# Optimization experiments

Hardware: AMD Instinct MI355X
Metric: run time of the kernel (lower is better)

The kernel has to match this reference:

```python
import jax, jax.numpy as jnp
import numpy as np

THETA = 10000.0
R_TOK = 4  # region_token_num


def _local_positions(regions, max_n):
    # 0-based position of each token within its region (count of prior tokens
    # with the same region id) -- order-based, works for any region layout.
    onehot = jax.nn.one_hot(regions, max_n + 1, dtype=jnp.int32)  # [B,T,N+1]
    counts = jnp.cumsum(onehot, axis=1)                            # inclusive
    return jnp.take_along_axis(counts, regions[..., None], axis=-1)[..., 0] - 1


def _rope(q, k, pos, theta):
    # full-head-dim rotary embedding, split-half convention
    D = q.shape[-1]
    inv_freq = 1.0 / (theta ** (jnp.arange(0, D, 2, dtype=jnp.float32) / D))  # [D/2]
    ang = pos[..., None].astype(jnp.float32) * inv_freq                        # [B,S,D/2]
    cos = jnp.tile(jnp.cos(ang), (1, 1, 2))[:, None]                           # [B,1,S,D]
    sin = jnp.tile(jnp.sin(ang), (1, 1, 2))[:, None]

    def rot(x):
        h = x.shape[-1] // 2
        return jnp.concatenate([-x[..., h:], x[..., :h]], axis=-1)

    return q * cos + rot(q) * sin, k * cos + rot(k) * sin


def setup_inputs() -> dict:
    B, H, D = 2, 16, 64
    T, MAX_N = 2048, 64
    P = MAX_N * R_TOK
    key = jax.random.key(0)
    ks = jax.random.split(key, 7)
    f = lambda k, s: jax.random.normal(k, s, dtype=jnp.float32)
    regions = jnp.sort(jax.random.randint(ks[6], (B, T), 1, MAX_N + 1, dtype=jnp.int32), axis=-1)
    return {
        'pool_q': f(ks[0], (B, H, P, D)),
        'pool_k': f(ks[1], (B, H, P, D)),
        'pool_v': f(ks[2], (B, H, P, D)),
        'x_q': f(ks[3], (B, H, T, D)),
        'x_k': f(ks[4], (B, H, T, D)),
        'x_v': f(ks[5], (B, H, T, D)),
        'regions': regions,
        't_mask': jnp.ones((B, T), dtype=bool),
        'n_mask': jnp.ones((B, MAX_N), dtype=bool),
        'max_n': MAX_N,
    }


def reference(pool_q, pool_k, pool_v, x_q, x_k, x_v, regions, t_mask, n_mask, max_n):
    B, H, P, D = pool_q.shape
    R = R_TOK
    # sequence = [pool, x]
    q = jnp.concatenate([pool_q, x_q], axis=2)
    k = jnp.concatenate([pool_k, x_k], axis=2)
    v = jnp.concatenate([pool_v, x_v], axis=2)

    # local-mode positions (use_pool_offset=False -> pool tokens at pos 0)
    pool_pos = jnp.zeros((B, P), dtype=jnp.int32)
    x_pos = (_local_positions(regions, max_n) + R) * (regions > 0).astype(jnp.int32)
    pos = jnp.concatenate([pool_pos, x_pos], axis=-1)  # [B,S]
    q, k = _rope(q, k, pos, THETA)

    # block-local (same-region) mask: [B,1,S,S], True = allowed
    pool_region = jnp.broadcast_to(jnp.repeat(jnp.arange(1, max_n + 1, dtype=jnp.int32), R)[None], (B, P))
    pool_valid = jnp.repeat(n_mask, R, axis=1)                      # [B,P]
    full_region = jnp.concatenate([pool_region, regions], axis=-1)  # [B,S]
    full_valid = jnp.concatenate([pool_valid, t_mask], axis=-1)     # [B,S]
    same = full_region[:, :, None] == full_region[:, None, :]
    valid = full_valid[:, :, None] & full_valid[:, None, :]
    nonpad = (full_region != 0)[:, :, None] & (full_region != 0)[:, None, :]
    mask = (same & valid & nonpad)[:, None]                          # [B,1,S,S]

    scores = jnp.einsum('bhqd,bhkd->bhqk', q, k) / jnp.sqrt(jnp.float32(D))
    scores = jnp.where(mask, scores, jnp.float32(-1e9))
    attn = jax.nn.softmax(scores, axis=-1)
    out = jnp.einsum('bhqk,bhkd->bhqd', attn, v)
    return out[:, :, :P, :]
```

## Files before the change

### kernel.cpp

```cpp
#include <hip/hip_runtime.h>

#define BB   2
#define HH   16
#define DD   64
#define TT   2048
#define MAXN 64
#define RTOK 4
#define PP   (MAXN * RTOK)
#define STR  72

typedef unsigned short u16x8 __attribute__((ext_vector_type(8)));
typedef unsigned short u16x4 __attribute__((ext_vector_type(4)));

__device__ __forceinline__ unsigned short f2bf(float f) {
    unsigned u = __float_as_uint(f);
    u += 0x7FFFu + ((u >> 16) & 1u);
    return (unsigned short)(u >> 16);
}
__device__ __forceinline__ float bf2f(unsigned short u) {
    return __uint_as_float(((unsigned int)u) << 16);
}

__global__ __launch_bounds__(256)
void build_ranges(const int* __restrict__ regions, int* __restrict__ tab) {
    const int b   = blockIdx.x;
    const int tid = threadIdx.x;
    const int* reg = regions + b * TT;
    int* t = tab + b * 66;
    const int i0 = tid * 8;
    int v[9];
    const int4 a0 = *(const int4*)(reg + i0);
    const int4 a1 = *(const int4*)(reg + i0 + 4);
    v[0] = a0.x; v[1] = a0.y; v[2] = a0.z; v[3] = a0.w;
    v[4] = a1.x; v[5] = a1.y; v[6] = a1.z; v[7] = a1.w;
    v[8] = (tid == 255) ? (MAXN + 1) : reg[i0 + 8];
    if (tid == 0)
        for (int rr = 1; rr <= v[0]; ++rr) t[rr] = 0;
    #pragma unroll
    for (int j = 0; j < 8; ++j)
        for (int rr = v[j] + 1; rr <= v[j + 1]; ++rr) t[rr] = i0 + j + 1;
}

__global__ __launch_bounds__(64, 2)
void lapd_attn(const float* __restrict__ pool_q,
               const float* __restrict__ pool_k,
               const float* __restrict__ pool_v,
               const float* __restrict__ x_k,
               const float* __restrict__ x_v,
               const int* __restrict__ tab,
               float* __restrict__ out) {
    const int blk   = blockIdx.x;
    const int r_idx = blk & (MAXN - 1);
    const int bh    = blk >> 6;
    const int b     = bh / HH;
    const int lane  = threadIdx.x;

    __shared__ __align__(16) unsigned short k_s16[64][STR];
    __shared__ __align__(16) unsigned short v_t16[64][STR];
    __shared__ __align__(16) unsigned short p_s16[4][STR];
    __shared__ float q_s[4][DD];

    const int* tb    = tab + b * 66;
    const int start  = tb[r_idx + 1];
    const int cnt    = tb[r_idx + 2] - start;
    const int sstart = (cnt > 0) ? start : 0;

    const size_t poolbase = ((size_t)bh * PP + r_idx * RTOK) * DD;
    const float* pk = pool_k + poolbase;
    const float* pv = pool_v + poolbase;
    const float* xk = x_k + (size_t)bh * TT * DD;
    const float* xv = x_v + (size_t)bh * TT * DD;

    const int qr = lane >> 4;
    const int qc = (lane & 15) * 4;
    {
        const float4 q4 = *(const float4*)(pool_q + poolbase + (size_t)(qr * DD) + qc);
        *(float4*)&q_s[qr][qc] =
            make_float4(q4.x * 0.125f, q4.y * 0.125f, q4.z * 0.125f, q4.w * 0.125f);
    }

    const int g = lane >> 3;
    const int d = (lane & 7) * 4;
    float invf[4];
    #pragma unroll
    for (int c = 0; c < 4; ++c)
        invf[c] = __expf((float)(d + c) * (-9.210340371976184f / 32.0f));

    float a0 = 0, a1 = 0, a2 = 0, a3 = 0, l = 0;
    int xbase = 0;
    bool first = true;

    for (;;) {
        const int koff = first ? RTOK : 0;
        int nx = cnt - xbase;
        if (nx > 64 - koff) nx = 64 - koff;
        if (nx < 0) nx = 0;
        const int tn = koff + nx;

        __syncthreads();

        #pragma unroll
        for (int ph = 0; ph < 4; ++ph) {
            const int keyA = ph * 16 + 2 * g;
            const int keyB = keyA + 1;
            int xiA = keyA - koff; if (xiA > nx - 1) xiA = nx - 1; if (xiA < 0) xiA = 0;
            int xiB = keyB - koff; if (xiB > nx - 1) xiB = nx - 1; if (xiB < 0) xiB = 0;
            const bool pA = first && (keyA < RTOK);
            const bool pB = first && (keyB < RTOK);
            const float* kbA = pA ? (pk + keyA * DD) : (xk + (size_t)(sstart + xbase + xiA) * DD);
            const float* vbA = pA ? (pv + keyA * DD) : (xv + (size_t)(sstart + xbase + xiA) * DD);
            const float* kbB = pB ? (pk + keyB * DD) : (xk + (size_t)(sstart + xbase + xiB) * DD);
            const float* vbB = pB ? (pv + keyB * DD) : (xv + (size_t)(sstart + xbase + xiB) * DD);
            const float4 kA0 = *(const float4*)(kbA + d);
            const float4 kA1 = *(const float4*)(kbA + d + 32);
            const float4 vA0 = *(const float4*)(vbA + d);
            const float4 vA1 = *(const float4*)(vbA + d + 32);
            const float4 kB0 = *(const float4*)(kbB + d);
            const float4 kB1 = *(const float4*)(kbB + d + 32);
            const float4 vB0 = *(const float4*)(vbB + d);
            const float4 vB1 = *(const float4*)(vbB + d + 32);

            {
                float lo0 = kA0.x, lo1 = kA0.y, lo2 = kA0.z, lo3 = kA0.w;
                float hi0 = kA1.x, hi1 = kA1.y, hi2 = kA1.z, hi3 = kA1.w;
                if (!pA) {
                    const float pos = (float)(xbase + xiA + RTOK);
                    float sv, cv;
                    __sincosf(pos * invf[0], &sv, &cv);
                    { const float L = lo0, H = hi0; lo0 = L*cv - H*sv; hi0 = H*cv + L*sv; }
                    __sincosf(pos * invf[1], &sv, &cv);
                    { const float L = lo1, H = hi1; lo1 = L*cv - H*sv; hi1 = H*cv + L*sv; }
                    __sincosf(pos * invf[2], &sv, &cv);
                    { const float L = lo2, H = hi2; lo2 = L*cv - H*sv; hi2 = H*cv + L*sv; }
                    __sincosf(pos * invf[3], &sv, &cv);
                    { const float L = lo3, H = hi3; lo3 = L*cv - H*sv; hi3 = H*cv + L*sv; }
                }
                u16x4 wlo = {f2bf(lo0), f2bf(lo1), f2bf(lo2), f2bf(lo3)};
                u16x4 whi = {f2bf(hi0), f2bf(hi1), f2bf(hi2), f2bf(hi3)};
                *(u16x4*)&k_s16[keyA][d]      = wlo;
                *(u16x4*)&k_s16[keyA][d + 32] = whi;
            }
            {
                float lo0 = kB0.x, lo1 = kB0.y, lo2 = kB0.z, lo3 = kB0.w;
                float hi0 = kB1.x, hi1 = kB1.y, hi2 = kB1.z, hi3 = kB1.w;
                if (!pB) {
                    const float pos = (float)(xbase + xiB + RTOK);
                    float sv, cv;
                    __sincosf(pos * invf[0], &sv, &cv);
                    { const float L = lo0, H = hi0; lo0 = L*cv - H*sv; hi0 = H*cv + L*sv; }
                    __sincosf(pos * invf[1], &sv, &cv);
                    { const float L = lo1, H = hi1; lo1 = L*cv - H*sv; hi1 = H*cv + L*sv; }
                    __sincosf(pos * invf[2], &sv, &cv);
                    { const float L = lo2, H = hi2; lo2 = L*cv - H*sv; hi2 = H*cv + L*sv; }
                    __sincosf(pos * invf[3], &sv, &cv);
                    { const float L = lo3, H = hi3; lo3 = L*cv - H*sv; hi3 = H*cv + L*sv; }
                }
                u16x4 wlo = {f2bf(lo0), f2bf(lo1), f2bf(lo2), f2bf(lo3)};
                u16x4 whi = {f2bf(hi0), f2bf(hi1), f2bf(hi2), f2bf(hi3)};
                *(u16x4*)&k_s16[keyB][d]      = wlo;
                *(u16x4*)&k_s16[keyB][d + 32] = whi;
            }
            {
                const unsigned w0 = (unsigned)f2bf(vA0.x) | ((unsigned)f2bf(vB0.x) << 16);
                const unsigned w1 = (unsigned)f2bf(vA0.y) | ((unsigned)f2bf(vB0.y) << 16);
                const unsigned w2 = (unsigned)f2bf(vA0.z) | ((unsigned)f2bf(vB0.z) << 16);
                const unsigned w3 = (unsigned)f2bf(vA0.w) | ((unsigned)f2bf(vB0.w) << 16);
                const unsigned h0 = (unsigned)f2bf(vA1.x) | ((unsigned)f2bf(vB1.x) << 16);
                const unsigned h1 = (unsigned)f2bf(vA1.y) | ((unsigned)f2bf(vB1.y) << 16);
                const unsigned h2 = (unsigned)f2bf(vA1.z) | ((unsigned)f2bf(vB1.z) << 16);
                const unsigned h3 = (unsigned)f2bf(vA1.w) | ((unsigned)f2bf(vB1.w) << 16);
                *(unsigned*)&v_t16[d + 0][keyA]      = w0;
                *(unsigned*)&v_t16[d + 1][keyA]      = w1;
                *(unsigned*)&v_t16[d + 2][keyA]      = w2;
                *(unsigned*)&v_t16[d + 3][keyA]      = w3;
                *(unsigned*)&v_t16[d + 32][keyA]     = h0;
                *(unsigned*)&v_t16[d + 33][keyA]     = h1;
                *(unsigned*)&v_t16[d + 34][keyA]     = h2;
                *(unsigned*)&v_t16[d + 35][keyA]     = h3;
            }
        }
        __syncthreads();

        float s0 = 0, s1 = 0, s2 = 0, s3 = 0;
        #pragma unroll
        for (int dd2 = 0; dd2 < DD; dd2 += 8) {
            const u16x8 kk = *(const u16x8*)&k_s16[lane][dd2];
            const float k0 = bf2f(kk[0]), k1 = bf2f(kk[1]), k2 = bf2f(kk[2]), k3 = bf2f(kk[3]);
            const float k4 = bf2f(kk[4]), k5 = bf2f(kk[5]), k6 = bf2f(kk[6]), k7 = bf2f(kk[7]);
            const float4 qa0 = *(const float4*)&q_s[0][dd2];
            const float4 qb0 = *(const float4*)&q_s[0][dd2 + 4];
            const float4 qa1 = *(const float4*)&q_s[1][dd2];
            const float4 qb1 = *(const float4*)&q_s[1][dd2 + 4];
            const float4 qa2 = *(const float4*)&q_s[2][dd2];
            const float4 qb2 = *(const float4*)&q_s[2][dd2 + 4];
            const float4 qa3 = *(const float4*)&q_s[3][dd2];
            const float4 qb3 = *(const float4*)&q_s[3][dd2 + 4];
            s0 += qa0.x*k0 + qa0.y*k1 + qa0.z*k2 + qa0.w*k3 + qb0.x*k4 + qb0.y*k5 + qb0.z*k6 + qb0.w*k7;
            s1 += qa1.x*k0 + qa1.y*k1 + qa1.z*k2 + qa1.w*k3 + qb1.x*k4 + qb1.y*k5 + qb1.z*k6 + qb1.w*k7;
            s2 += qa2.x*k0 + qa2.y*k1 + qa2.z*k2 + qa2.w*k3 + qb2.x*k4 + qb2.y*k5 + qb2.z*k6 + qb2.w*k7;
            s3 += qa3.x*k0 + qa3.y*k1 + qa3.z*k2 + qa3.w*k3 + qb3.x*k4 + qb3.y*k5 + qb3.z*k6 + qb3.w*k7;
        }
        const bool ok = (lane < tn);
        p_s16[0][lane] = f2bf(ok ? __expf(s0) : 0.0f);
        p_s16[1][lane] = f2bf(ok ? __expf(s1) : 0.0f);
        p_s16[2][lane] = f2bf(ok ? __expf(s2) : 0.0f);
        p_s16[3][lane] = f2bf(ok ? __expf(s3) : 0.0f);
        __syncthreads();

        #pragma unroll
        for (int k = 0; k < 64; k += 8) {
            const u16x8 pp = *(const u16x8*)&p_s16[qr][k];
            const float p0 = bf2f(pp[0]), p1 = bf2f(pp[1]), p2 = bf2f(pp[2]), p3 = bf2f(pp[3]);
            const float p4 = bf2f(pp[4]), p5 = bf2f(pp[5]), p6 = bf2f(pp[6]), p7 = bf2f(pp[7]);
            const u16x8 w0 = *(const u16x8*)&v_t16[qc + 0][k];
            const u16x8 w1 = *(const u16x8*)&v_t16[qc + 1][k];
            const u16x8 w2 = *(const u16x8*)&v_t16[qc + 2][k];
            const u16x8 w3 = *(const u16x8*)&v_t16[qc + 3][k];
            a0 += p0*bf2f(w0[0]) + p1*bf2f(w0[1]) + p2*bf2f(w0[2]) + p3*bf2f(w0[3])
                + p4*bf2f(w0[4]) + p5*bf2f(w0[5]) + p6*bf2f(w0[6]) + p7*bf2f(w0[7]);
            a1 += p0*bf2f(w1[0]) + p1*bf2f(w1[1]) + p2*bf2f(w1[2]) + p3*bf2f(w1[3])
                + p4*bf2f(w1[4]) + p5*bf2f(w1[5]) + p6*bf2f(w1[6]) + p7*bf2f(w1[7]);
            a2 += p0*bf2f(w2[0]) + p1*bf2f(w2[1]) + p2*bf2f(w2[2]) + p3*bf2f(w2[3])
                + p4*bf2f(w2[4]) + p5*bf2f(w2[5]) + p6*bf2f(w2[6]) + p7*bf2f(w2[7]);
            a3 += p0*bf2f(w3[0]) + p1*bf2f(w3[1]) + p2*bf2f(w3[2]) + p3*bf2f(w3[3])
                + p4*bf2f(w3[4]) + p5*bf2f(w3[5]) + p6*bf2f(w3[6]) + p7*bf2f(w3[7]);
            l  += ((p0 + p1) + (p2 + p3)) + ((p4 + p5) + (p6 + p7));
        }

        xbase += nx;
        first = false;
        if (xbase >= cnt) break;
    }

    const float rl = 1.0f / l;
    *(float4*)(out + poolbase + (size_t)(qr * DD) + qc) =
        make_float4(a0 * rl, a1 * rl, a2 * rl, a3 * rl);
}

extern "C" void kernel_launch(void* const* d_in, const int* in_sizes, int n_in,
                              void* d_out, int out_size, void* d_ws, size_t ws_size,
                              hipStream_t stream) {
    const float* pool_q  = (const float*)d_in[0];
    const float* pool_k  = (const float*)d_in[1];
    const float* pool_v  = (const float*)d_in[2];
    const float* x_k     = (const float*)d_in[4];
    const float* x_v     = (const float*)d_in[5];
    const int*   regions = (const int*)d_in[6];
    float*       out     = (float*)d_out;
    int*         tab     = (int*)d_ws;

    build_ranges<<<dim3(BB), dim3(256), 0, stream>>>(regions, tab);
    lapd_attn<<<dim3(BB * HH * MAXN), dim3(64), 0, stream>>>(
        pool_q, pool_k, pool_v, x_k, x_v, tab, out);
}
```

Before: 110.8 us.

## Split region attention across two waves and skip empty key chunks

Each block now runs two waves of 64 lanes instead of one. Key and value loading is split so each wave handles half of the 64-key chunk. The QK dot product is split across half-lanes over the head dimension and combined with a shuffle. The PV loop runs only up to the rounded-up valid key count, and each thread produces two output columns instead of four. This aims to cut per-thread serial work and skip padding keys, since regions average about 32 tokens. The cost is an extra shuffle and a larger block.

Result: faster. 107.8 us (-2.8%).

```diff
diff --git a/kernel.cpp b/kernel.cpp
--- a/kernel.cpp
+++ b/kernel.cpp
@@ -41,7 +41,7 @@
         for (int rr = v[j] + 1; rr <= v[j + 1]; ++rr) t[rr] = i0 + j + 1;
 }
 
-__global__ __launch_bounds__(64, 2)
+__global__ __launch_bounds__(128, 4)
 void lapd_attn(const float* __restrict__ pool_q,
                const float* __restrict__ pool_k,
                const float* __restrict__ pool_v,
@@ -53,7 +53,9 @@
     const int r_idx = blk & (MAXN - 1);
     const int bh    = blk >> 6;
     const int b     = bh / HH;
-    const int lane  = threadIdx.x;
+    const int tid   = threadIdx.x;
+    const int wave  = tid >> 6;
+    const int lane  = tid & 63;
 
     __shared__ __align__(16) unsigned short k_s16[64][STR];
     __shared__ __align__(16) unsigned short v_t16[64][STR];
@@ -71,11 +73,10 @@
     const float* xk = x_k + (size_t)bh * TT * DD;
     const float* xv = x_v + (size_t)bh * TT * DD;
 
-    const int qr = lane >> 4;
-    const int qc = (lane & 15) * 4;
     {
-        const float4 q4 = *(const float4*)(pool_q + poolbase + (size_t)(qr * DD) + qc);
-        *(float4*)&q_s[qr][qc] =
+        const int r = lane >> 4, c = (lane & 15) * 4;
+        const float4 q4 = *(const float4*)(pool_q + poolbase + (size_t)(r * DD) + c);
+        *(float4*)&q_s[r][c] =
             make_float4(q4.x * 0.125f, q4.y * 0.125f, q4.z * 0.125f, q4.w * 0.125f);
     }
 
@@ -86,7 +87,12 @@
     for (int c = 0; c < 4; ++c)
         invf[c] = __expf((float)(d + c) * (-9.210340371976184f / 32.0f));
 
-    float a0 = 0, a1 = 0, a2 = 0, a3 = 0, l = 0;
+    const int sk = lane & 31;
+    const int h  = lane >> 5;
+    const int row = 2 * wave + (lane >> 5);
+    const int dp  = (lane & 31) * 2;
+
+    float accA = 0.0f, accB = 0.0f, l = 0.0f;
     int xbase = 0;
     bool first = true;
 
@@ -95,136 +101,142 @@
         int nx = cnt - xbase;
         if (nx > 64 - koff) nx = 64 - koff;
         if (nx < 0) nx = 0;
-        const int tn = koff + nx;
+        const int tn   = koff + nx;
+        const int kmax = (tn + 7) & ~7;
 
         __syncthreads();
 
         #pragma unroll
-        for (int ph = 0; ph < 4; ++ph) {
-            const int keyA = ph * 16 + 2 * g;
-            const int keyB = keyA + 1;
-            int xiA = keyA - koff; if (xiA > nx - 1) xiA = nx - 1; if (xiA < 0) xiA = 0;
-            int xiB = keyB - koff; if (xiB > nx - 1) xiB = nx - 1; if (xiB < 0) xiB = 0;
-            const bool pA = first && (keyA < RTOK);
-            const bool pB = first && (keyB < RTOK);
-            const float* kbA = pA ? (pk + keyA * DD) : (xk + (size_t)(sstart + xbase + xiA) * DD);
-            const float* vbA = pA ? (pv + keyA * DD) : (xv + (size_t)(sstart + xbase + xiA) * DD);
-            const float* kbB = pB ? (pk + keyB * DD) : (xk + (size_t)(sstart + xbase + xiB) * DD);
-            const float* vbB = pB ? (pv + keyB * DD) : (xv + (size_t)(sstart + xbase + xiB) * DD);
-            const float4 kA0 = *(const float4*)(kbA + d);
-            const float4 kA1 = *(const float4*)(kbA + d + 32);
-            const float4 vA0 = *(const float4*)(vbA + d);
-            const float4 vA1 = *(const float4*)(vbA + d + 32);
-            const float4 kB0 = *(const float4*)(kbB + d);
-            const float4 kB1 = *(const float4*)(kbB + d + 32);
-            const float4 vB0 = *(const float4*)(vbB + d);
-            const float4 vB1 = *(const float4*)(vbB + d + 32);
-
-            {
-                float lo0 = kA0.x, lo1 = kA0.y, lo2 = kA0.z, lo3 = kA0.w;
-                float hi0 = kA1.x, hi1 = kA1.y, hi2 = kA1.z, hi3 = kA1.w;
-                if (!pA) {
-                    const float pos = (float)(xbase + xiA + RTOK);
-                    float sv, cv;
-                    __sincosf(pos * invf[0], &sv, &cv);
-                    { const float L = lo0, H = hi0; lo0 = L*cv - H*sv; hi0 = H*cv + L*sv; }
-                    __sincosf(pos * invf[1], &sv, &cv);
-                    { const float L = lo1, H = hi1; lo1 = L*cv - H*sv; hi1 = H*cv + L*sv; }
-                    __sincosf(pos * invf[2], &sv, &cv);
-                    { const float L = lo2, H = hi2; lo2 = L*cv - H*sv; hi2 = H*cv + L*sv; }
-                    __sincosf(pos * invf[3], &sv, &cv);
-                    { const float L = lo3, H = hi3; lo3 = L*cv - H*sv; hi3 = H*cv + L*sv; }
+        for (int ph = 0; ph < 2; ++ph) {
+            const int base = 32 * wave + 16 * ph;
+            if (base < tn) {
+                const int keyA = base + 2 * g;
+                const int keyB = keyA + 1;
+                int xiA = keyA - koff; if (xiA > nx - 1) xiA = nx - 1; if (xiA < 0) xiA = 0;
+                int xiB = keyB - koff; if (xiB > nx - 1) xiB = nx - 1; if (xiB < 0) xiB = 0;
+                const bool pA = first && (keyA < RTOK);
+                const bool pB = first && (keyB < RTOK);
+                const float* kbA = pA ? (pk + keyA * DD) : (xk + (size_t)(sstart + xbase + xiA) * DD);
+                const float* vbA = pA ? (pv + keyA * DD) : (xv + (size_t)(sstart + xbase + xiA) * DD);
+                const float* kbB = pB ? (pk + keyB * DD) : (xk + (size_t)(sstart + xbase + xiB) * DD);
+                const float* vbB = pB ? (pv + keyB * DD) : (xv + (size_t)(sstart + xbase + xiB) * DD);
+                const float4 kA0 = *(const float4*)(kbA + d);
+                const float4 kA1 = *(const float4*)(kbA + d + 32);
+                const float4 vA0 = *(const float4*)(vbA + d);
+                const float4 vA1 = *(const float4*)(vbA + d + 32);
+                const float4 kB0 = *(const float4*)(kbB + d);
+                const float4 kB1 = *(const float4*)(kbB + d + 32);
+                const float4 vB0 = *(const float4*)(vbB + d);
+                const float4 vB1 = *(const float4*)(vbB + d + 32);
+
+                {
+                    float lo0 = kA0.x, lo1 = kA0.y, lo2 = kA0.z, lo3 = kA0.w;
+                    float hi0 = kA1.x, hi1 = kA1.y, hi2 = kA1.z, hi3 = kA1.w;
+                    if (!pA) {
+                        const float pos = (float)(xbase + xiA + RTOK);
+                        float sv, cv;
+                        __sincosf(pos * invf[0], &sv, &cv);
+                        { const float L = lo0, H = hi0; lo0 = L*cv - H*sv; hi0 = H*cv + L*sv; }
+                        __sincosf(pos * invf[1], &sv, &cv);
+                        { const float L = lo1, H = hi1; lo1 = L*cv - H*sv; hi1 = H*cv + L*sv; }
+                        __sincosf(pos * invf[2], &sv, &cv);
+                        { const float L = lo2, H = hi2; lo2 = L*cv - H*sv; hi2 = H*cv + L*sv; }
+                        __sincosf(pos * invf[3], &sv, &cv);
+                        { const float L = lo3, H = hi3; lo3 = L*cv - H*sv; hi3 = H*cv + L*sv; }
+                    }
+                    u16x4 wlo = {f2bf(lo0), f2bf(lo1), f2bf(lo2), f2bf(lo3)};
+                    u16x4 whi = {f2bf(hi0), f2bf(hi1), f2bf(hi2), f2bf(hi3)};
+                    *(u16x4*)&k_s16[keyA][d]      = wlo;
+                    *(u16x4*)&k_s16[keyA][d + 32] = whi;
                 }
-                u16x4 wlo = {f2bf(lo0), f2bf(lo1), f2bf(lo2), f2bf(lo3)};
-                u16x4 whi = {f2bf(hi0), f2bf(hi1), f2bf(hi2), f2bf(hi3)};
-                *(u16x4*)&k_s16[keyA][d]      = wlo;
-                *(u16x4*)&k_s16[keyA][d + 32] = whi;
+                {
+                    float lo0 = kB0.x, lo1 = kB0.y, lo2 = kB0.z, lo3 = kB0.w;
+                    float hi0 = kB1.x, hi1 = kB1.y, hi2 = kB1.z, hi3 = kB1.w;
+                    if (!pB) {
+                        const float pos = (float)(xbase + xiB + RTOK);
+                        float sv, cv;
+                        __sincosf(pos * invf[0], &sv, &cv);
+                        { const float L = lo0, H = hi0; lo0 = L*cv - H*sv; hi0 = H*cv + L*sv; }
+                        __sincosf(pos * invf[1], &sv, &cv);
+                        { const float L = lo1, H = hi1; lo1 = L*cv - H*sv; hi1 = H*cv + L*sv; }
+                        __sincosf(pos * invf[2], &sv, &cv);
+                        { const float L = lo2, H = hi2; lo2 = L*cv - H*sv; hi2 = H*cv + L*sv; }
+                        __sincosf(pos * invf[3], &sv, &cv);
+                        { const float L = lo3, H = hi3; lo3 = L*cv - H*sv; hi3 = H*cv + L*sv; }
+                    }
+                    u16x4 wlo = {f2bf(lo0), f2bf(lo1), f2bf(lo2), f2bf(lo3)};
+                    u16x4 whi = {f2bf(hi0), f2bf(hi1), f2bf(hi2), f2bf(hi3)};
+                    *(u16x4*)&k_s16[keyB][d]      = wlo;
+                    *(u16x4*)&k_s16[keyB][d + 32] = whi;
+                }
+                {
+                    const unsigned w0 = (unsigned)f2bf(vA0.x) | ((unsigned)f2bf(vB0.x) << 16);
+                    const unsigned w1 = (unsigned)f2bf(vA0.y) | ((unsigned)f2bf(vB0.y) << 16);
+                    const unsigned w2 = (unsigned)f2bf(vA0.z) | ((unsigned)f2bf(vB0.z) << 16);
+                    const unsigned w3 = (unsigned)f2bf(vA0.w) | ((unsigned)f2bf(vB0.w) << 16);
+                    const unsigned h0 = (unsigned)f2bf(vA1.x) | ((unsigned)f2bf(vB1.x) << 16);
+                    const unsigned h1 = (unsigned)f2bf(vA1.y) | ((unsigned)f2bf(vB1.y) << 16);
+                    const unsigned h2 = (unsigned)f2bf(vA1.z) | ((unsigned)f2bf(vB1.z) << 16);
+                    const unsigned h3 = (unsigned)f2bf(vA1.w) | ((unsigned)f2bf(vB1.w) << 16);
+                    *(unsigned*)&v_t16[d + 0][keyA]  = w0;
+                    *(unsigned*)&v_t16[d + 1][keyA]  = w1;
+                    *(unsigned*)&v_t16[d + 2][keyA]  = w2;
+                    *(unsigned*)&v_t16[d + 3][keyA]  = w3;
+                    *(unsigned*)&v_t16[d + 32][keyA] = h0;
+                    *(unsigned*)&v_t16[d + 33][keyA] = h1;
+                    *(unsigned*)&v_t16[d + 34][keyA] = h2;
+                    *(unsigned*)&v_t16[d + 35][keyA] = h3;
+                }
             }
-            {
-                float lo0 = kB0.x, lo1 = kB0.y, lo2 = kB0.z, lo3 = kB0.w;
-                float hi0 = kB1.x, hi1 = kB1.y, hi2 = kB1.z, hi3 = kB1.w;
-                if (!pB) {
-                    const float pos = (float)(xbase + xiB + RTOK);
-                    float sv, cv;
-                    __sincosf(pos * invf[0], &sv, &cv);
-                    { const float L = lo0, H = hi0; lo0 = L*cv - H*sv; hi0 = H*cv + L*sv; }
-                    __sincosf(pos * invf[1], &sv, &cv);
-                    { const float L = lo1, H = hi1; lo1 = L*cv - H*sv; hi1 = H*cv + L*sv; }
-                    __sincosf(pos * invf[2], &sv, &cv);
-                    { const float L = lo2, H = hi2; lo2 = L*cv - H*sv; hi2 = H*cv + L*sv; }
-                    __sincosf(pos * invf[3], &sv, &cv);
-                    { const float L = lo3, H = hi3; lo3 = L*cv - H*sv; hi3 = H*cv + L*sv; }
-                }
-                u16x4 wlo = {f2bf(lo0), f2bf(lo1), f2bf(lo2), f2bf(lo3)};
-                u16x4 whi = {f2bf(hi0), f2bf(hi1), f2bf(hi2), f2bf(hi3)};
-                *(u16x4*)&k_s16[keyB][d]      = wlo;
-                *(u16x4*)&k_s16[keyB][d + 32] = whi;
+        }
+
+        if (32 * wave < tn) {
+            const int key = 32 * wave + sk;
+            const int d0  = h * 32;
+            float s0 = 0, s1 = 0, s2 = 0, s3 = 0;
+            #pragma unroll
+            for (int dd2 = 0; dd2 < 32; dd2 += 8) {
+                const u16x8 kk = *(const u16x8*)&k_s16[key][d0 + dd2];
+                const float k0 = bf2f(kk[0]), k1 = bf2f(kk[1]), k2 = bf2f(kk[2]), k3 = bf2f(kk[3]);
+                const float k4 = bf2f(kk[4]), k5 = bf2f(kk[5]), k6 = bf2f(kk[6]), k7 = bf2f(kk[7]);
+                const float4 qa0 = *(const float4*)&q_s[0][d0 + dd2];
+                const float4 qb0 = *(const float4*)&q_s[0][d0 + dd2 + 4];
+                const float4 qa1 = *(const float4*)&q_s[1][d0 + dd2];
+                const float4 qb1 = *(const float4*)&q_s[1][d0 + dd2 + 4];
+                const float4 qa2 = *(const float4*)&q_s[2][d0 + dd2];
+                const float4 qb2 = *(const float4*)&q_s[2][d0 + dd2 + 4];
+                const float4 qa3 = *(const float4*)&q_s[3][d0 + dd2];
+                const float4 qb3 = *(const float4*)&q_s[3][d0 + dd2 + 4];
+                s0 += qa0.x*k0 + qa0.y*k1 + qa0.z*k2 + qa0.w*k3 + qb0.x*k4 + qb0.y*k5 + qb0.z*k6 + qb0.w*k7;
+                s1 += qa1.x*k0 + qa1.y*k1 + qa1.z*k2 + qa1.w*k3 + qb1.x*k4 + qb1.y*k5 + qb1.z*k6 + qb1.w*k7;
+                s2 += qa2.x*k0 + qa2.y*k1 + qa2.z*k2 + qa2.w*k3 + qb2.x*k4 + qb2.y*k5 + qb2.z*k6 + qb2.w*k7;
+                s3 += qa3.x*k0 + qa3.y*k1 + qa3.z*k2 + qa3.w*k3 + qb3.x*k4 + qb3.y*k5 + qb3.z*k6 + qb3.w*k7;
             }
-            {
-                const unsigned w0 = (unsigned)f2bf(vA0.x) | ((unsigned)f2bf(vB0.x) << 16);
-                const unsigned w1 = (unsigned)f2bf(vA0.y) | ((unsigned)f2bf(vB0.y) << 16);
-                const unsigned w2 = (unsigned)f2bf(vA0.z) | ((unsigned)f2bf(vB0.z) << 16);
-                const unsigned w3 = (unsigned)f2bf(vA0.w) | ((unsigned)f2bf(vB0.w) << 16);
-                const unsigned h0 = (unsigned)f2bf(vA1.x) | ((unsigned)f2bf(vB1.x) << 16);
-                const unsigned h1 = (unsigned)f2bf(vA1.y) | ((unsigned)f2bf(vB1.y) << 16);
-                const unsigned h2 = (unsigned)f2bf(vA1.z) | ((unsigned)f2bf(vB1.z) << 16);
-                const unsigned h3 = (unsigned)f2bf(vA1.w) | ((unsigned)f2bf(vB1.w) << 16);
-                *(unsigned*)&v_t16[d + 0][keyA]      = w0;
-                *(unsigned*)&v_t16[d + 1][keyA]      = w1;
-                *(unsigned*)&v_t16[d + 2][keyA]      = w2;
-                *(unsigned*)&v_t16[d + 3][keyA]      = w3;
-                *(unsigned*)&v_t16[d + 32][keyA]     = h0;
-                *(unsigned*)&v_t16[d + 33][keyA]     = h1;
-                *(unsigned*)&v_t16[d + 34][keyA]     = h2;
-                *(unsigned*)&v_t16[d + 35][keyA]     = h3;
+            s0 += __shfl_xor(s0, 32, 64);
+            s1 += __shfl_xor(s1, 32, 64);
+            s2 += __shfl_xor(s2, 32, 64);
+            s3 += __shfl_xor(s3, 32, 64);
+            if (h == 0) {
+                const bool ok = (key < tn);
+                p_s16[0][key] = f2bf(ok ? __expf(s0) : 0.0f);
+                p_s16[1][key] = f2bf(ok ? __expf(s1) : 0.0f);
+                p_s16[2][key] = f2bf(ok ? __expf(s2) : 0.0f);
+                p_s16[3][key] = f2bf(ok ? __expf(s3) : 0.0f);
             }
         }
         __syncthreads();
 
-        float s0 = 0, s1 = 0, s2 = 0, s3 = 0;
-        #pragma unroll
-        for (int dd2 = 0; dd2 < DD; dd2 += 8) {
-            const u16x8 kk = *(const u16x8*)&k_s16[lane][dd2];
-            const float k0 = bf2f(kk[0]), k1 = bf2f(kk[1]), k2 = bf2f(kk[2]), k3 = bf2f(kk[3]);
-            const float k4 = bf2f(kk[4]), k5 = bf2f(kk[5]), k6 = bf2f(kk[6]), k7 = bf2f(kk[7]);
-            const float4 qa0 = *(const float4*)&q_s[0][dd2];
-            const float4 qb0 = *(const float4*)&q_s[0][dd2 + 4];
-            const float4 qa1 = *(const float4*)&q_s[1][dd2];
-            const float4 qb1 = *(const float4*)&q_s[1][dd2 + 4];
-            const float4 qa2 = *(const float4*)&q_s[2][dd2];
-            const float4 qb2 = *(const float4*)&q_s[2][dd2 + 4];
-            const float4 qa3 = *(const float4*)&q_s[3][dd2];
-            const float4 qb3 = *(const float4*)&q_s[3][dd2 + 4];
-            s0 += qa0.x*k0 + qa0.y*k1 + qa0.z*k2 + qa0.w*k3 + qb0.x*k4 + qb0.y*k5 + qb0.z*k6 + qb0.w*k7;
-            s1 += qa1.x*k0 + qa1.y*k1 + qa1.z*k2 + qa1.w*k3 + qb1.x*k4 + qb1.y*k5 + qb1.z*k6 + qb1.w*k7;
-            s2 += qa2.x*k0 + qa2.y*k1 + qa2.z*k2 + qa2.w*k3 + qb2.x*k4 + qb2.y*k5 + qb2.z*k6 + qb2.w*k7;
-            s3 += qa3.x*k0 + qa3.y*k1 + qa3.z*k2 + qa3.w*k3 + qb3.x*k4 + qb3.y*k5 + qb3.z*k6 + qb3.w*k7;
-        }
-        const bool ok = (lane < tn);
-        p_s16[0][lane] = f2bf(ok ? __expf(s0) : 0.0f);
-        p_s16[1][lane] = f2bf(ok ? __expf(s1) : 0.0f);
-        p_s16[2][lane] = f2bf(ok ? __expf(s2) : 0.0f);
-        p_s16[3][lane] = f2bf(ok ? __expf(s3) : 0.0f);
-        __syncthreads();
-
-        #pragma unroll
-        for (int k = 0; k < 64; k += 8) {
-            const u16x8 pp = *(const u16x8*)&p_s16[qr][k];
+        for (int k = 0; k < kmax; k += 8) {
+            const u16x8 pp = *(const u16x8*)&p_s16[row][k];
+            const u16x8 w0 = *(const u16x8*)&v_t16[dp][k];
+            const u16x8 w1 = *(const u16x8*)&v_t16[dp + 1][k];
             const float p0 = bf2f(pp[0]), p1 = bf2f(pp[1]), p2 = bf2f(pp[2]), p3 = bf2f(pp[3]);
             const float p4 = bf2f(pp[4]), p5 = bf2f(pp[5]), p6 = bf2f(pp[6]), p7 = bf2f(pp[7]);
-            const u16x8 w0 = *(const u16x8*)&v_t16[qc + 0][k];
-            const u16x8 w1 = *(const u16x8*)&v_t16[qc + 1][k];
-            const u16x8 w2 = *(const u16x8*)&v_t16[qc + 2][k];
-            const u16x8 w3 = *(const u16x8*)&v_t16[qc + 3][k];
-            a0 += p0*bf2f(w0[0]) + p1*bf2f(w0[1]) + p2*bf2f(w0[2]) + p3*bf2f(w0[3])
-                + p4*bf2f(w0[4]) + p5*bf2f(w0[5]) + p6*bf2f(w0[6]) + p7*bf2f(w0[7]);
-            a1 += p0*bf2f(w1[0]) + p1*bf2f(w1[1]) + p2*bf2f(w1[2]) + p3*bf2f(w1[3])
-                + p4*bf2f(w1[4]) + p5*bf2f(w1[5]) + p6*bf2f(w1[6]) + p7*bf2f(w1[7]);
-            a2 += p0*bf2f(w2[0]) + p1*bf2f(w2[1]) + p2*bf2f(w2[2]) + p3*bf2f(w2[3])
-                + p4*bf2f(w2[4]) + p5*bf2f(w2[5]) + p6*bf2f(w2[6]) + p7*bf2f(w2[7]);
-            a3 += p0*bf2f(w3[0]) + p1*bf2f(w3[1]) + p2*bf2f(w3[2]) + p3*bf2f(w3[3])
-                + p4*bf2f(w3[4]) + p5*bf2f(w3[5]) + p6*bf2f(w3[6]) + p7*bf2f(w3[7]);
-            l  += ((p0 + p1) + (p2 + p3)) + ((p4 + p5) + (p6 + p7));
+            accA += p0*bf2f(w0[0]) + p1*bf2f(w0[1]) + p2*bf2f(w0[2]) + p3*bf2f(w0[3])
+                  + p4*bf2f(w0[4]) + p5*bf2f(w0[5]) + p6*bf2f(w0[6]) + p7*bf2f(w0[7]);
+            accB += p0*bf2f(w1[0]) + p1*bf2f(w1[1]) + p2*bf2f(w1[2]) + p3*bf2f(w1[3])
+                  + p4*bf2f(w1[4]) + p5*bf2f(w1[5]) + p6*bf2f(w1[6]) + p7*bf2f(w1[7]);
+            l    += ((p0 + p1) + (p2 + p3)) + ((p4 + p5) + (p6 + p7));
         }
 
         xbase += nx;
@@ -233,8 +245,7 @@
     }
 
     const float rl = 1.0f / l;
-    *(float4*)(out + poolbase + (size_t)(qr * DD) + qc) =
-        make_float4(a0 * rl, a1 * rl, a2 * rl, a3 * rl);
+    *(float2*)(out + poolbase + (size_t)(row * DD) + dp) = make_float2(accA * rl, accB * rl);
 }
 
 extern "C" void kernel_launch(void* const* d_in, const int* in_sizes, int n_in,
@@ -250,6 +261,6 @@
     int*         tab     = (int*)d_ws;
 
     build_ranges<<<dim3(BB), dim3(256), 0, stream>>>(regions, tab);
-    lapd_attn<<<dim3(BB * HH * MAXN), dim3(64), 0, stream>>>(
+    lapd_attn<<<dim3(BB * HH * MAXN), dim3(128), 0, stream>>>(
         pool_q, pool_k, pool_v, x_k, x_v, tab, out);
 }
```
